# Performance work log

Measured on AMD Instinct MI355X. Metric: run time of the kernel, lower is better.

## Reference

```python
import math
import numpy as np
import jax, jax.numpy as jnp

C = 8  # hidden multiplicity (num_channels)
B, N = 4, 4096

# ---------- real Wigner 3j (e3nn convention: Frobenius norm 1) ----------

def _su2_cg(l1, l2, l3):
    f = math.factorial
    def cg(m1, m2, m3):
        if m1 + m2 != m3:
            return 0.0
        pref = math.sqrt((2 * l3 + 1) * f(l3 + l1 - l2) * f(l3 - l1 + l2) * f(l1 + l2 - l3) / f(l1 + l2 + l3 + 1))
        pref *= math.sqrt(f(l3 + m3) * f(l3 - m3) * f(l1 - m1) * f(l1 + m1) * f(l2 - m2) * f(l2 + m2))
        s = 0.0
        for k in range(l1 + l2 - l3 + 1):
            d = [k, l1 + l2 - l3 - k, l1 - m1 - k, l2 + m2 - k, l3 - l2 + m1 + k, l3 - l1 - m2 + k]
            if min(d) < 0:
                continue
            s += (-1.0) ** k / np.prod([float(f(x)) for x in d])
        return pref * s
    out = np.zeros((2 * l1 + 1, 2 * l2 + 1, 2 * l3 + 1))
    for i, m1 in enumerate(range(-l1, l1 + 1)):
        for j, m2 in enumerate(range(-l2, l2 + 1)):
            for k, m3 in enumerate(range(-l3, l3 + 1)):
                out[i, j, k] = cg(m1, m2, m3)
    return out

def _q_real_to_complex(l):
    q = np.zeros((2 * l + 1, 2 * l + 1), dtype=np.complex128)
    rs2 = 1.0 / math.sqrt(2.0)
    for m in range(-l, 0):
        q[l + m, l + abs(m)] = rs2
        q[l + m, l - abs(m)] = -1j * rs2
    q[l, l] = 1.0
    for m in range(1, l + 1):
        q[l + m, l + abs(m)] = (-1) ** m * rs2
        q[l + m, l - abs(m)] = 1j * (-1) ** m * rs2
    return (-1j) ** l * q

def _w3j(l1, l2, l3):
    Q1, Q2, Q3 = _q_real_to_complex(l1), _q_real_to_complex(l2), _q_real_to_complex(l3)
    Cc = _su2_cg(l1, l2, l3).astype(np.complex128)
    Cr = np.real(np.einsum('ij,kl,mn,ikm->jln', Q1, Q2, np.conj(Q3), Cc))
    return (Cr / np.linalg.norm(Cr)).astype(np.float32)

# tensor-product paths (selection rules for 4e/6e inputs, 0e/2e SH, 4e/6e outputs)
VAL_PATHS = [(4, 0, 4), (4, 2, 4), (6, 2, 4), (4, 2, 6), (6, 0, 6), (6, 2, 6)]
OUT_PATHS = [(4, 4, 4), (4, 6, 4), (6, 4, 4), (6, 6, 4), (4, 4, 6), (4, 6, 6), (6, 4, 6), (6, 6, 6)]
# path normalization ('element'): fan-in = 3*C for tp_val outputs, 4*C^2 for tp_out outputs
W3J_VAL = [jnp.asarray(_w3j(*p) * math.sqrt((2 * p[2] + 1) / (3.0 * C))) for p in VAL_PATHS]
W3J_OUT = [jnp.asarray(_w3j(*p) * math.sqrt((2 * p[2] + 1) / (4.0 * C * C))) for p in OUT_PATHS]


def _forward(feat, sh_lr, log_s, pos_w, pos_b, w_lin_in, w_val, w_out, w_lin_out):
    b, n, _ = feat.shape
    f4, f6 = feat[..., :9], feat[..., 9:]                      # 1x4e, 1x6e
    f4n = f4 / jnp.maximum(jnp.linalg.norm(f4, axis=-1, keepdims=True), 1e-12)
    f6n = f6 / jnp.maximum(jnp.linalg.norm(f6, axis=-1, keepdims=True), 1e-12)
    s4, s6 = jnp.exp(log_s[0]), jnp.exp(log_s[1])
    scores = s4 * jnp.einsum('bnd,bmd->bnm', f4n, f4n) + s6 * jnp.einsum('bnd,bmd->bnm', f6n, f6n)
    pb = sh_lr @ pos_w + pos_b                                 # (N,)
    scores = scores + (pb[:, None] + pb[None, :])[None]
    attn = jax.nn.softmax(scores.astype(jnp.float32), axis=-1).astype(feat.dtype)

    h4 = f4[:, :, None, :] * w_lin_in[0][None, None, :, None]  # (B,N,C,9)
    h6 = f6[:, :, None, :] * w_lin_in[1][None, None, :, None]  # (B,N,C,13)

    y = {0: sh_lr[:, :1], 2: sh_lr[:, 1:]}                     # (N,1), (N,5)
    hx = {4: h4, 6: h6}
    v = {4: jnp.zeros((b, n, C, 9), feat.dtype), 6: jnp.zeros((b, n, C, 13), feat.dtype)}
    for p, (l1, l2, l3) in enumerate(VAL_PATHS):
        v[l3] = v[l3] + jnp.einsum('bnui,nj,ijk,uw->bnwk', hx[l1], y[l2], W3J_VAL[p], w_val[p])
    vals = jnp.concatenate([v[4].reshape(b, n, 9 * C), v[6].reshape(b, n, 13 * C)], axis=-1)

    ctx = jnp.einsum('bnm,bmd->bnd', attn, vals)               # (B,N,22C)
    cx = {4: ctx[..., :9 * C].reshape(b, n, C, 9), 6: ctx[..., 9 * C:].reshape(b, n, C, 13)}
    o = {4: jnp.zeros((b, n, C, 9), feat.dtype), 6: jnp.zeros((b, n, C, 13), feat.dtype)}
    for p, (l1, l2, l3) in enumerate(OUT_PATHS):
        o[l3] = o[l3] + jnp.einsum('bnui,bnvj,ijk,uvw->bnwk', hx[l1], cx[l2], W3J_OUT[p], w_out[p])

    inv_sc = 1.0 / math.sqrt(C)                                # lin_out fan_in = C
    d4 = jnp.einsum('bnui,u->bni', o[4], w_lin_out[0]) * inv_sc
    d6 = jnp.einsum('bnui,u->bni', o[6], w_lin_out[1]) * inv_sc
    return jnp.concatenate([d4, d6], axis=-1)                  # (B,N,22)


def setup_inputs() -> dict:
    key = jax.random.key(0)
    ks = jax.random.split(key, 8)
    feat = jax.random.normal(ks[0], (B, N, 22), jnp.float32)
    sh_lr = jax.random.normal(ks[1], (N, 6), jnp.float32)
    log_s = jnp.array([math.log(1.0 / 3.0), math.log(1.0 / math.sqrt(13.0))], jnp.float32)
    pos_w = 0.01 * jax.random.normal(ks[2], (6,), jnp.float32)
    pos_b = jnp.zeros((), jnp.float32)
    w_lin_in = jax.random.normal(ks[3], (2, C), jnp.float32)
    w_val = jax.random.normal(ks[4], (6, C, C), jnp.float32)
    w_out = jax.random.normal(ks[5], (8, C, C, C), jnp.float32)
    w_lin_out = jax.random.normal(ks[6], (2, C), jnp.float32)
    return dict(feat=feat, sh_lr=sh_lr, log_s=log_s, pos_w=pos_w, pos_b=pos_b,
                w_lin_in=w_lin_in, w_val=w_val, w_out=w_out, w_lin_out=w_lin_out)


def reference(feat, sh_lr, log_s, pos_w, pos_b, w_lin_in, w_val, w_out, w_lin_out):
    return _forward(feat, sh_lr, log_s, pos_w, pos_b, w_lin_in, w_val, w_out, w_lin_out)
```

## Files before the change

kernel.cpp:

```cpp
#include <hip/hip_runtime.h>
#include <cmath>

#define NN 4096
#define BB 4
#define CCH 8

#define OFF_W3JVAL 0
#define OFF_W3JOUT 2688
#define OFF_CTX0   13568
#define CTXS       1572864
#define OFFB_KGH   25220096ULL
#define OFFB_KGL   26268672ULL
#define OFFB_VG    27317248ULL
#define OFFB_WBH   30462976ULL
#define OFFB_WBL   30493696ULL

typedef short s16x8 __attribute__((ext_vector_type(8)));
typedef _Float16 f16x8 __attribute__((ext_vector_type(8)));
typedef float f32x4 __attribute__((ext_vector_type(4)));
typedef unsigned int u32x4 __attribute__((ext_vector_type(4)));
typedef unsigned int u32x2 __attribute__((ext_vector_type(2)));

static __device__ __forceinline__ unsigned short f2bf(float x){
  unsigned u = __float_as_uint(x);
  return (unsigned short)((u + 0x7FFFu + ((u >> 16) & 1u)) >> 16);
}
static __device__ __forceinline__ float bf2f(unsigned short h){
  return __uint_as_float(((unsigned)h) << 16);
}
static __device__ __forceinline__ unsigned pk2r(float v){
  unsigned short h = f2bf(v);
  unsigned short l = f2bf(v - bf2f(h));
  return ((unsigned)l << 16) | (unsigned)h;
}
static __device__ __forceinline__ unsigned short f2h(float x){
  return __builtin_bit_cast(unsigned short, (_Float16)x);
}
static __device__ __forceinline__ void unpk(u32x4 a, u32x4 b, s16x8& h, s16x8& l){
  u32x4 hw = { __builtin_amdgcn_perm(a[1],a[0],0x05040100u),
               __builtin_amdgcn_perm(a[3],a[2],0x05040100u),
               __builtin_amdgcn_perm(b[1],b[0],0x05040100u),
               __builtin_amdgcn_perm(b[3],b[2],0x05040100u)};
  u32x4 lw = { __builtin_amdgcn_perm(a[1],a[0],0x07060302u),
               __builtin_amdgcn_perm(a[3],a[2],0x07060302u),
               __builtin_amdgcn_perm(b[1],b[0],0x07060302u),
               __builtin_amdgcn_perm(b[3],b[2],0x07060302u)};
  h = __builtin_bit_cast(s16x8, hw);
  l = __builtin_bit_cast(s16x8, lw);
}

static __device__ __forceinline__ void qentf(int l, int r, int c, float& re, float& im){
  re=0.f; im=0.f;
  float s = ((l&3)==2)? -1.f : 1.f;
  const float rs2 = 0.70710678118654752440f;
  if(r < l){
    if(c == 2*l - r) re = s*rs2;
    else if(c == r)  im = -s*rs2;
  } else if(r == l){
    if(c == l) re = s;
  } else {
    float sg = ((r-l)&1)? -1.f : 1.f;
    if(c == r) re = s*sg*rs2;
    else if(c == 2*l - r) im = s*sg*rs2;
  }
}
__global__ __launch_bounds__(512) void k_tab(float* __restrict__ Wv, float* __restrict__ Wo){
  __shared__ float Ccf[2197];
  __shared__ float red[512];
  __shared__ double factS[20];
  int t = threadIdx.x;
  int p = blockIdx.x;
  if(t==0){
    double f=1.0; factS[0]=1.0;
    for(int i=1;i<20;i++){ f*=(double)i; factS[i]=f; }
  }
  const int L1[14]={4,4,6,4,6,6, 4,4,6,6,4,4,6,6};
  const int L2[14]={0,2,2,2,0,2, 4,6,4,6,4,6,4,6};
  const int L3[14]={4,4,4,6,6,6, 4,4,4,4,6,6,6,6};
  const int OFF[14]={0,81,486,1071,1656,1825, 0,729,1782,2835,4356,5409,6930,8451};
  int l1=L1[p], l2=L2[p], l3=L3[p];
  int d1=2*l1+1, d2=2*l2+1, d3=2*l3+1;
  int tot = d1*d2*d3;
  float* dst = (p<6) ? (Wv+OFF[p]) : (Wo+OFF[p]);
  float scale = (p<6) ? sqrtf((2.f*l3+1.f)/24.f) : sqrtf((2.f*l3+1.f)/256.f);
  __syncthreads();
  #pragma unroll 1
  for(int e=t; e<tot; e+=512){
    int i = e/(d2*d3), rem = e - i*(d2*d3), j = rem/d3, k = rem - j*d3;
    int m1=i-l1, m2=j-l2, m3=k-l3;
    double v=0.0;
    if(m1+m2==m3){
      double pref = sqrt((2.0*l3+1.0)*factS[l3+l1-l2]*factS[l3-l1+l2]*factS[l1+l2-l3]/factS[l1+l2+l3+1]);
      pref *= sqrt(factS[l3+m3]*factS[l3-m3]*factS[l1-m1]*factS[l1+m1]*factS[l2-m2]*factS[l2+m2]);
      double s=0.0;
      #pragma unroll 1
      for(int kk=0; kk<=l1+l2-l3; kk++){
        int dd0=kk, dd1=l1+l2-l3-kk, dd2=l1-m1-kk, dd3=l2+m2-kk, dd4=l3-l2+m1+kk, dd5=l3-l1-m2+kk;
        int mn=dd0;
        if(dd1<mn)mn=dd1; if(dd2<mn)mn=dd2; if(dd3<mn)mn=dd3; if(dd4<mn)mn=dd4; if(dd5<mn)mn=dd5;
        if(mn<0) continue;
        double prod = factS[dd0]*factS[dd1]*factS[dd2]*factS[dd3]*factS[dd4]*factS[dd5];
        s += ((kk&1)? -1.0:1.0)/prod;
      }
      v = pref*s;
    }
    Ccf[e]=(float)v;
  }
  __syncthreads();
  float nacc=0.f;
  #pragma unroll 1
  for(int e=t; e<tot; e+=512){
    int j = e/(d2*d3), rem = e - j*(d2*d3), l = rem/d3, n = rem - l*d3;
    float re = 0.f;
    #pragma unroll
    for(int ii=0; ii<2; ii++){
      int i = ii ? (2*l1 - j) : j;
      float q1r,q1i; qentf(l1,i,j,q1r,q1i);
      if(ii && i==j){ q1r=0.f; q1i=0.f; }
      #pragma unroll
      for(int kk=0; kk<2; kk++){
        int k = kk ? (2*l2 - l) : l;
        float q2r,q2i; qentf(l2,k,l,q2r,q2i);
        if(kk && k==l){ q2r=0.f; q2i=0.f; }
        float ar = q1r*q2r - q1i*q2i;
        float ai = q1r*q2i + q1i*q2r;
        #pragma unroll
        for(int mm=0; mm<2; mm++){
          int m = mm ? (2*l3 - n) : n;
          float q3r,q3i; qentf(l3,m,n,q3r,q3i);
          if(mm && m==n){ q3r=0.f; q3i=0.f; }
          float coef = ar*q3r + ai*q3i;
          re = fmaf(coef, Ccf[(i*d2+k)*d3+m], re);
        }
      }
    }
    dst[e]=re;
    nacc = fmaf(re,re,nacc);
  }
  red[t]=nacc;
  __syncthreads();
  #pragma unroll 1
  for(int s=256;s>0;s>>=1){
    if(t<s) red[t]+=red[t+s];
    __syncthreads();
  }
  float c = scale/sqrtf(red[0]);
  #pragma unroll 1
  for(int e=t; e<tot; e+=512) dst[e]*=c;
}

__global__ void k_weights(const float* __restrict__ wli, const float* __restrict__ wval,
                          const float* __restrict__ wout, const float* __restrict__ wlo,
                          const float* __restrict__ Wv,
                          unsigned short* __restrict__ WBH, unsigned short* __restrict__ WBL){
  __shared__ float bws[48];
  __shared__ float scs[64];
  __shared__ float As[24];
  int t = threadIdx.x;
  if(t<48){
    const int val_l1[6]={0,0,1,0,1,1};
    int p=t>>3, w=t&7;
    float s=0.f;
    for(int u=0;u<8;u++) s = fmaf(wli[val_l1[p]*8+u], wval[(p*8+u)*8+w], s);
    bws[t]=s;
  }
  {
    const int out_l1[8]={0,0,1,1,0,0,1,1};
    const int out_l3[8]={0,0,0,0,1,1,1,1};
    int p=t>>3, v=t&7;
    float s=0.f;
    for(int u=0;u<8;u++){
      float a=wli[out_l1[p]*8+u];
      for(int w=0;w<8;w++) s = fmaf(wout[((p*8+u)*8+v)*8+w]*a, wlo[out_l3[p]*8+w], s);
    }
    scs[t]=s*0.35355339059327373f;
  }
  __syncthreads();
  if(t<24){
    int p=t/3, i3=t-3*p;
    int vp = (p&1)*3 + i3;
    float s=0.f;
    for(int w=0;w<8;w++) s = fmaf(scs[p*8+w], bws[vp*8+w], s);
    As[t]=s;
  }
  __syncthreads();
  int base = blockIdx.x*960;
  for(int k=0;k<15;k++){
    int cell = base + k*64 + t;
    int f = cell/160, c = cell - f*160;
    float v = 0.f;
    if(f < 88 && c < 132){
      int seg = f/22, off = f - seg*22;
      int even = (off < 9);
      int p = 2*seg + (even?0:1);
      int jo = even ? off : off-9;
      int l1, i, jj;
      if(c < 54){ l1=4; i=c/6; jj=c-6*i; }
      else { int cc=c-54; l1=6; i=cc/6; jj=cc-6*i; }
      if(even){
        if(l1==4 && jj==0)      v = As[p*3+0]*Wv[i*9+jo];
        else if(l1==4)          v = As[p*3+1]*Wv[81+(i*5+jj-1)*9+jo];
        else if(jj>=1)          v = As[p*3+2]*Wv[486+(i*5+jj-1)*9+jo];
      } else {
        if(l1==4 && jj>=1)      v = As[p*3+0]*Wv[1071+(i*5+jj-1)*13+jo];
        else if(l1==6 && jj==0) v = As[p*3+1]*Wv[1656+i*13+jo];
        else if(l1==6)          v = As[p*3+2]*Wv[1825+(i*5+jj-1)*13+jo];
      }
    } else if(f==88 && c==132){
      v = 1.0f;
    }
    unsigned short h = f2bf(v);
    WBH[cell] = h;
    WBL[cell] = f2bf(v - bf2f(h));
  }
}

__launch_bounds__(128)
__global__ void k_prep(const float* __restrict__ feat, const float* __restrict__ sh,
                       const float* __restrict__ log_s, const float* __restrict__ pos_w,
                       const float* __restrict__ pos_b,
                       const unsigned short* __restrict__ WBH,
                       const unsigned short* __restrict__ WBL,
                       unsigned short* __restrict__ Kgh, unsigned short* __restrict__ Kgl,
                       unsigned short* __restrict__ Vg){
  __shared__ __align__(16) unsigned int Pbuf[16*164];
  __shared__ unsigned int Po[96*17];
  __shared__ float epbs[16];
  int tid = threadIdx.x;
  int w2 = tid >> 6, lane = tid & 63;
  int lm = lane & 15, quad = lane >> 4;
  int seg = w2*4 + quad;
  int panel = blockIdx.x >> 2, mt = blockIdx.x & 3;
  int idxp = panel*64 + mt*16 + lm;
  int n = idxp & (NN-1);
  const float* fp = feat + (size_t)idxp*22;
  const float* shp = sh + n*6;
  float f[22];
  #pragma unroll
  for(int c=0;c<22;c++) f[c]=fp[c];
  float y[6];
  #pragma unroll
  for(int j=0;j<6;j++) y[j]=shp[j];
  if(tid<16){
    float pb = pos_b[0];
    #pragma unroll
    for(int j=0;j<6;j++) pb = fmaf(y[j], pos_w[j], pb);
    epbs[lm] = __expf(pb);
    float n4=0.f, n6=0.f;
    #pragma unroll
    for(int c=0;c<9;c++) n4 += f[c]*f[c];
    #pragma unroll
    for(int c=9;c<22;c++) n6 += f[c]*f[c];
    n4 = fmaxf(sqrtf(n4), 1e-12f);
    n6 = fmaxf(sqrtf(n6), 1e-12f);
    float s4 = __expf(log_s[0]), s6 = __expf(log_s[1]);
    float a4 = sqrtf(s4)/n4, a6 = sqrtf(s6)/n6;
    unsigned short* kph = Kgh + (size_t)idxp*32;
    unsigned short* kpl = Kgl + (size_t)idxp*32;
    #pragma unroll
    for(int c=0;c<22;c++){
      float qv = f[c] * (c<9 ? a4 : a6);
      unsigned short h = f2bf(qv);
      kph[c]=h; kpl[c]=f2bf(qv - bf2f(h));
    }
    #pragma unroll
    for(int c=22;c<32;c++){ kph[c]=0; kpl[c]=0; }
  }
  #pragma unroll
  for(int j4=0;j4<5;j4++){
    u32x4 wv;
    #pragma unroll
    for(int e=0;e<4;e++){
      int c = seg*20 + j4*4 + e;
      float pv;
      if(c<54){ int i=c/6, jj=c-6*i; pv = f[i]*y[jj]; }
      else if(c<132){ int cc=c-54; int i=cc/6, jj=cc-6*i; pv = f[9+i]*y[jj]; }
      else if(c==132) pv = 1.0f;
      else pv = 0.0f;
      wv[e] = pk2r(pv);
    }
    *(u32x4*)&Pbuf[lm*164 + seg*20 + j4*4] = wv;
  }
  __syncthreads();
  f32x4 acc[3];
  #pragma unroll
  for(int ft=0;ft<3;ft++)
    #pragma unroll
    for(int i=0;i<4;i++) acc[ft][i]=0.f;
  for(int kc=0;kc<5;kc++){
    const u32x4* ap = (const u32x4*)&Pbuf[lm*164 + kc*32 + quad*8];
    s16x8 Ah, Al;
    unpk(ap[0], ap[1], Ah, Al);
    #pragma unroll
    for(int ft=0;ft<3;ft++){
      int ftg = w2*3 + ft;
      size_t bo = (size_t)(ftg*16+lm)*160 + kc*32 + quad*8;
      s16x8 Bh = *(const s16x8*)(WBH + bo);
      s16x8 Bl = *(const s16x8*)(WBL + bo);
      f32x4 a = acc[ft];
      a = __builtin_amdgcn_mfma_f32_16x16x32_bf16(Al, Bl, a, 0,0,0);
      a = __builtin_amdgcn_mfma_f32_16x16x32_bf16(Al, Bh, a, 0,0,0);
      a = __builtin_amdgcn_mfma_f32_16x16x32_bf16(Ah, Bl, a, 0,0,0);
      a = __builtin_amdgcn_mfma_f32_16x16x32_bf16(Ah, Bh, a, 0,0,0);
      acc[ft] = a;
    }
  }
  #pragma unroll
  for(int r=0;r<4;r++){
    float e = epbs[quad*4 + r];
    #pragma unroll
    for(int ft=0;ft<3;ft++){
      int ftg = w2*3 + ft;
      Po[(ftg*16+lm)*17 + quad*4 + r] = (unsigned)f2h(acc[ft][r]*e);
    }
  }
  __syncthreads();
  unsigned int* vO32 = (unsigned int*)(Vg + (size_t)panel*96*64);
  #pragma unroll
  for(int wv=0; wv<6; wv++){
    int idx2 = wv*128 + tid;
    int g = idx2 >> 3, j = idx2 & 7;
    unsigned lo = Po[g*17 + 2*j] & 0xFFFFu;
    unsigned hi = Po[g*17 + 2*j + 1] & 0xFFFFu;
    vO32[g*32 + mt*8 + j] = lo | (hi<<16);
  }
}

#define LDSK  0
#define LDSKL 4096
#define LDSV  8192
#define BUFB  20480
__global__ __launch_bounds__(512)
__attribute__((amdgpu_waves_per_eu(4, 4)))
void k_attn(const unsigned short* __restrict__ Kgh,
            const unsigned short* __restrict__ Kgl,
            const unsigned short* __restrict__ Vg,
            float* __restrict__ ctx0){
  __shared__ __align__(16) unsigned char lds[73728];
  int tid = threadIdx.x;
  int lane = tid & 63, w = tid >> 6;
  int lm = lane & 15, quad = lane >> 4;
  int blk = blockIdx.x;
  int b = blk & 3, kh = (blk>>2)&3, qb = blk >> 4;
  const unsigned short* KhB = Kgh + (size_t)b*NN*32;
  const unsigned short* KlB = Kgl + (size_t)b*NN*32;
  const unsigned short* VB  = Vg  + (size_t)b*64*96*64;
  float* ctx = ctx0 + (size_t)kh*CTXS + (size_t)b*NN*96;
  int qrow = qb*128 + w*16 + lm;

  s16x8 qh, ql;
  { size_t ro = (size_t)qrow*32 + (size_t)quad*8;
    qh = *(const s16x8*)(KhB + ro);
    ql = *(const s16x8*)(KlB + ro); }

  int kro = lm*64 + ((quad ^ ((lm>>1)&3))<<4);
  int vr0 = lm*128 + (((0*4+quad) ^ (lm&7))<<4);
  int vr1 = lm*128 + (((1*4+quad) ^ (lm&7))<<4);

  int dofs[3], sofs[3], sreg[3];
  #pragma unroll
  for(int rep=0;rep<3;rep++){
    int g = tid + 512*rep;
    if(g < 512){
      int gk = g & 255;
      int row = gk>>2, col = gk&3;
      int t = row>>4, rr = row&15;
      int kact = 32*(t&1) + 8*(rr>>2) + 4*(t>>1) + (rr&3);
      sreg[rep] = (g<256)? 0 : 1;
      sofs[rep] = kact*64 + col*16;
      dofs[rep] = ((g<256)? LDSK : LDSKL) + row*64 + ((col ^ ((row>>1)&3))<<4);
    }
    else if(g < 1280){ int gv=g-512; sreg[rep]=2; sofs[rep]=gv*16;
      dofs[rep] = LDSV + (gv>>3)*128 + (((gv&7) ^ ((gv>>3)&7))<<4); }
    else { sreg[rep]=-1; sofs[rep]=0; dofs[rep]=0; }
  }

  f32x4 acc[6];
  #pragma unroll
  for(int ft=0;ft<6;ft++)
    #pragma unroll
    for(int i=0;i<4;i++) acc[ft][i]=0.f;

  u32x4 stg0, stg1, stg2;

#define MFB(A,Bv,C) __builtin_amdgcn_mfma_f32_16x16x32_bf16(A,Bv,C,0,0,0)
#define MFH(A,Bv,C) __builtin_amdgcn_mfma_f32_16x16x32_f16(A,Bv,C,0,0,0)

#define STG_ISSUE(T) { \
  const char* kb_ = (const char*)(KhB + (size_t)(kh*16+(T))*2048); \
  const char* lb_ = (const char*)(KlB + (size_t)(kh*16+(T))*2048); \
  const char* vb_ = (const char*)(VB  + (size_t)(kh*16+(T))*6144); \
  { const char* sp_ = (sreg[0]==0)? kb_ : (sreg[0]==1)? lb_ : vb_; \
    stg0 = *(const u32x4*)(sp_ + sofs[0]); } \
  { const char* sp_ = (sreg[1]==0)? kb_ : (sreg[1]==1)? lb_ : vb_; \
    stg1 = *(const u32x4*)(sp_ + sofs[1]); } \
  if(sreg[2]>=0){ stg2 = *(const u32x4*)(vb_ + sofs[2]); } }

#define STG_WRITE(BN) { \
  *(u32x4*)&lds[(BN)*BUFB + dofs[0]] = stg0; \
  *(u32x4*)&lds[(BN)*BUFB + dofs[1]] = stg1; \
  if(sreg[2]>=0){ *(u32x4*)&lds[(BN)*BUFB + dofs[2]] = stg2; } }

#define COMPUTE(B) { \
  unsigned Wt[4][2]; \
  _Pragma("unroll") \
  for(int kt=0;kt<4;kt++){ \
    s16x8 kfh = *(const s16x8*)&lds[(B)*BUFB + LDSK  + kt*1024 + kro]; \
    s16x8 kfl = *(const s16x8*)&lds[(B)*BUFB + LDSKL + kt*1024 + kro]; \
    f32x4 s_ = {0.f,0.f,0.f,0.f}; \
    s_ = MFB(kfl, qh, s_); \
    s_ = MFB(kfh, ql, s_); \
    s_ = MFB(kfh, qh, s_); \
    Wt[kt][0] = (unsigned)f2h(__expf(s_[0])) | ((unsigned)f2h(__expf(s_[1]))<<16); \
    Wt[kt][1] = (unsigned)f2h(__expf(s_[2])) | ((unsigned)f2h(__expf(s_[3]))<<16); \
  } \
  _Pragma("unroll") \
  for(int c=0;c<2;c++){ \
    u32x4 paw = {Wt[c][0], Wt[c][1], Wt[c+2][0], Wt[c+2][1]}; \
    f16x8 PA = __builtin_bit_cast(f16x8, paw); \
    int vro_ = c ? vr1 : vr0; \
    _Pragma("unroll") \
    for(int ft=0;ft<6;ft++){ \
      f16x8 vf = *(const f16x8*)&lds[(B)*BUFB + LDSV + ft*2048 + vro_]; \
      acc[ft] = MFH(PA, vf, acc[ft]); } \
  } }

  STG_ISSUE(0);
  STG_WRITE(0);
  __syncthreads();

  #pragma unroll 1
  for(int tp=0; tp<8; tp++){
    int t0 = 2*tp;
    STG_ISSUE(t0+1);
    COMPUTE(0);
    STG_WRITE(1);
    __syncthreads();
    if(t0+2 < 16){ STG_ISSUE(t0+2); }
    COMPUTE(1);
    if(t0+2 < 16){ STG_WRITE(0); }
    __syncthreads();
  }

#undef MFB
#undef MFH
#undef STG_ISSUE
#undef STG_WRITE
#undef COMPUTE

  #pragma unroll
  for(int ft=0;ft<6;ft++){
    int col = ft*16 + lm;
    #pragma unroll
    for(int r=0;r<4;r++){
      int row = qb*128 + w*16 + quad*4 + r;
      ctx[(size_t)row*96 + col] = acc[ft][r];
    }
  }
}

__launch_bounds__(256, 4)
__global__ void k_out(const float* __restrict__ feat, const float* __restrict__ ctxA,
                      const float* __restrict__ w3jout, float* __restrict__ out){
  __shared__ float gbuf[16*45];
  __shared__ float fbuf[16*24];
  __shared__ float dls[4*64*13];
  __shared__ float inv[16];
  int tid = threadIdx.x;
  int typ = blockIdx.x & 1;
  int n0 = (blockIdx.x>>1)*16;
  int gc0 = typ*44;
  for(int i=tid;i<16*44;i+=256){
    int pt=i/44, c=i-pt*44;
    const float* base = ctxA + (size_t)(n0+pt)*96 + gc0 + c;
    gbuf[pt*45+c] = base[0]+base[CTXS]+base[2*CTXS]+base[3*CTXS];
  }
  for(int i=tid;i<16*22;i+=256){
    int pt=i/22, c=i-pt*22;
    fbuf[pt*24+c] = feat[(size_t)(n0+pt)*22+c];
  }
  if(tid<16){
    const float* bd = ctxA + (size_t)(n0+tid)*96 + 88;
    inv[tid] = 1.0f/(bd[0]+bd[CTXS]+bd[2*CTXS]+bd[3*CTXS]);
  }
  __syncthreads();
  int lane = tid&63, w = tid>>6;
  int pt = lane&15, sub = lane>>4;
  float fR[13], gR[13], d[13];
  {
    int FB = (w&2)?9:0;
    int fn = (w&2)?13:9;
    #pragma unroll 13
    for(int i=0;i<13;i++) fR[i] = (i<fn) ? fbuf[pt*24 + FB + i] : 0.f;
    int GBl = (w==0)?0:(w==1)?9:(w==2)?22:31;
    int jn = (w&1)?13:9;
    #pragma unroll 13
    for(int j=0;j<13;j++) gR[j] = (j<jn) ? gbuf[pt*45 + GBl + j] : 0.f;
  }
  #pragma unroll 13
  for(int k=0;k<13;k++) d[k]=0.f;

#define PATHR(ID,JD,KD,WO) \
  _Pragma("unroll") \
  for(int ii=0;ii<((ID)+3)/4;ii++){ int i=sub+4*ii; if(i<(ID)){ float fv=fR[i]; \
    _Pragma("unroll") \
    for(int j=0;j<(JD);j++){ float val=fv*gR[j]; \
      const float* wp = w3jout + (WO) + (i*(JD)+j)*(KD); \
      _Pragma("unroll") \
      for(int k=0;k<(KD);k++) d[k] = fmaf(val, wp[k], d[k]); } } }

  int pcase = typ*4 + w;
  switch(pcase){
    case 0: PATHR(9,9,9, 0)       break;
    case 1: PATHR(9,13,9, 729)    break;
    case 2: PATHR(13,9,9, 1782)   break;
    case 3: PATHR(13,13,9, 2835)  break;
    case 4: PATHR(9,9,13, 4356)   break;
    case 5: PATHR(9,13,13, 5409)  break;
    case 6: PATHR(13,9,13, 6930)  break;
    default:PATHR(13,13,13, 8451) break;
  }
#undef PATHR
  {
    float* dp = &dls[(w*64+lane)*13];
    #pragma unroll 13
    for(int k=0;k<13;k++) dp[k]=d[k];
  }
  __syncthreads();
  {
    int KD = typ?13:9;
    int kb = typ?9:0;
    int pt2 = tid&15, kc = tid>>4;
    if(kc < KD){
      float s = 0.f;
      #pragma unroll
      for(int ww=0;ww<4;ww++)
        #pragma unroll
        for(int ss=0;ss<4;ss++)
          s += dls[(ww*64 + ss*16 + pt2)*13 + kc];
      out[(size_t)(n0+pt2)*22 + kb + kc] = s*inv[pt2];
    }
  }
}

extern "C" void kernel_launch(void* const* d_in, const int* in_sizes, int n_in,
                              void* d_out, int out_size, void* d_ws, size_t ws_size,
                              hipStream_t stream){
  (void)in_sizes; (void)n_in; (void)out_size; (void)ws_size;
  const float* feat =(const float*)d_in[0];
  const float* sh   =(const float*)d_in[1];
  const float* log_s=(const float*)d_in[2];
  const float* pos_w=(const float*)d_in[3];
  const float* pos_b=(const float*)d_in[4];
  const float* wli  =(const float*)d_in[5];
  const float* wval =(const float*)d_in[6];
  const float* wout =(const float*)d_in[7];
  const float* wlo  =(const float*)d_in[8];
  float* outp=(float*)d_out;
  float* wsf=(float*)d_ws;

  unsigned short* Kgh=(unsigned short*)((char*)d_ws + OFFB_KGH);
  unsigned short* Kgl=(unsigned short*)((char*)d_ws + OFFB_KGL);
  unsigned short* Vg =(unsigned short*)((char*)d_ws + OFFB_VG);
  unsigned short* WBH=(unsigned short*)((char*)d_ws + OFFB_WBH);
  unsigned short* WBL=(unsigned short*)((char*)d_ws + OFFB_WBL);

  hipLaunchKernelGGL(k_tab, dim3(14), dim3(512), 0, stream,
                     wsf+OFF_W3JVAL, wsf+OFF_W3JOUT);
  hipLaunchKernelGGL(k_weights, dim3(16), dim3(64), 0, stream,
                     wli, wval, wout, wlo, wsf+OFF_W3JVAL, WBH, WBL);
  hipLaunchKernelGGL(k_prep, dim3(1024), dim3(128), 0, stream,
                     feat, sh, log_s, pos_w, pos_b, WBH, WBL,
                     Kgh, Kgl, Vg);
  hipLaunchKernelGGL(k_attn, dim3(512), dim3(512), 0, stream,
                     Kgh, Kgl, Vg, wsf+OFF_CTX0);
  hipLaunchKernelGGL(k_out, dim3(2048), dim3(256), 0, stream,
                     feat, wsf+OFF_CTX0, wsf+OFF_W3JOUT, outp);
}
```

Before: 177.8 us.

## Process two query tiles per wave in attention kernel to reuse staged K/V

Each wave now handles 32 query rows (two 16-row tiles) instead of 16. The K and V fragments loaded from LDS are reused across both tiles, and the grid is halved to 256 blocks, so global-to-LDS staging traffic per query is halved. Accumulator and register use roughly doubles, so the occupancy hint drops from 4 to 2 waves per EU. The LDS allocation is also trimmed to the two buffers actually used. The cost is lower occupancy and fewer blocks to spread across the CUs.

Result: no change. 176.8 us (-0.6%).

```diff
diff --git a/kernel.cpp b/kernel.cpp
--- a/kernel.cpp
+++ b/kernel.cpp
@@ -331,12 +331,12 @@
 #define LDSV  8192
 #define BUFB  20480
 __global__ __launch_bounds__(512)
-__attribute__((amdgpu_waves_per_eu(4, 4)))
+__attribute__((amdgpu_waves_per_eu(2, 2)))
 void k_attn(const unsigned short* __restrict__ Kgh,
             const unsigned short* __restrict__ Kgl,
             const unsigned short* __restrict__ Vg,
             float* __restrict__ ctx0){
-  __shared__ __align__(16) unsigned char lds[73728];
+  __shared__ __align__(16) unsigned char lds[2*BUFB];
   int tid = threadIdx.x;
   int lane = tid & 63, w = tid >> 6;
   int lm = lane & 15, quad = lane >> 4;
@@ -346,12 +346,14 @@
   const unsigned short* KlB = Kgl + (size_t)b*NN*32;
   const unsigned short* VB  = Vg  + (size_t)b*64*96*64;
   float* ctx = ctx0 + (size_t)kh*CTXS + (size_t)b*NN*96;
-  int qrow = qb*128 + w*16 + lm;
-
-  s16x8 qh, ql;
-  { size_t ro = (size_t)qrow*32 + (size_t)quad*8;
-    qh = *(const s16x8*)(KhB + ro);
-    ql = *(const s16x8*)(KlB + ro); }
+
+  s16x8 qh[2], ql[2];
+  #pragma unroll
+  for(int q2=0;q2<2;q2++){
+    size_t ro = (size_t)(qb*256 + w*32 + q2*16 + lm)*32 + (size_t)quad*8;
+    qh[q2] = *(const s16x8*)(KhB + ro);
+    ql[q2] = *(const s16x8*)(KlB + ro);
+  }
 
   int kro = lm*64 + ((quad ^ ((lm>>1)&3))<<4);
   int vr0 = lm*128 + (((0*4+quad) ^ (lm&7))<<4);
@@ -375,11 +377,13 @@
     else { sreg[rep]=-1; sofs[rep]=0; dofs[rep]=0; }
   }
 
-  f32x4 acc[6];
-  #pragma unroll
-  for(int ft=0;ft<6;ft++)
-    #pragma unroll
-    for(int i=0;i<4;i++) acc[ft][i]=0.f;
+  f32x4 acc[2][6];
+  #pragma unroll
+  for(int q2=0;q2<2;q2++)
+    #pragma unroll
+    for(int ft=0;ft<6;ft++)
+      #pragma unroll
+      for(int i=0;i<4;i++) acc[q2][ft][i]=0.f;
 
   u32x4 stg0, stg1, stg2;
 
@@ -402,27 +406,33 @@
   if(sreg[2]>=0){ *(u32x4*)&lds[(BN)*BUFB + dofs[2]] = stg2; } }
 
 #define COMPUTE(B) { \
-  unsigned Wt[4][2]; \
+  unsigned Wt[2][4][2]; \
   _Pragma("unroll") \
   for(int kt=0;kt<4;kt++){ \
     s16x8 kfh = *(const s16x8*)&lds[(B)*BUFB + LDSK  + kt*1024 + kro]; \
     s16x8 kfl = *(const s16x8*)&lds[(B)*BUFB + LDSKL + kt*1024 + kro]; \
-    f32x4 s_ = {0.f,0.f,0.f,0.f}; \
-    s_ = MFB(kfl, qh, s_); \
-    s_ = MFB(kfh, ql, s_); \
-    s_ = MFB(kfh, qh, s_); \
-    Wt[kt][0] = (unsigned)f2h(__expf(s_[0])) | ((unsigned)f2h(__expf(s_[1]))<<16); \
-    Wt[kt][1] = (unsigned)f2h(__expf(s_[2])) | ((unsigned)f2h(__expf(s_[3]))<<16); \
+    _Pragma("unroll") \
+    for(int q2=0;q2<2;q2++){ \
+      f32x4 s_ = {0.f,0.f,0.f,0.f}; \
+      s_ = MFB(kfl, qh[q2], s_); \
+      s_ = MFB(kfh, ql[q2], s_); \
+      s_ = MFB(kfh, qh[q2], s_); \
+      Wt[q2][kt][0] = (unsigned)f2h(__expf(s_[0])) | ((unsigned)f2h(__expf(s_[1]))<<16); \
+      Wt[q2][kt][1] = (unsigned)f2h(__expf(s_[2])) | ((unsigned)f2h(__expf(s_[3]))<<16); \
+    } \
   } \
   _Pragma("unroll") \
   for(int c=0;c<2;c++){ \
-    u32x4 paw = {Wt[c][0], Wt[c][1], Wt[c+2][0], Wt[c+2][1]}; \
-    f16x8 PA = __builtin_bit_cast(f16x8, paw); \
+    u32x4 paw0 = {Wt[0][c][0], Wt[0][c][1], Wt[0][c+2][0], Wt[0][c+2][1]}; \
+    u32x4 paw1 = {Wt[1][c][0], Wt[1][c][1], Wt[1][c+2][0], Wt[1][c+2][1]}; \
+    f16x8 PA0 = __builtin_bit_cast(f16x8, paw0); \
+    f16x8 PA1 = __builtin_bit_cast(f16x8, paw1); \
     int vro_ = c ? vr1 : vr0; \
     _Pragma("unroll") \
     for(int ft=0;ft<6;ft++){ \
       f16x8 vf = *(const f16x8*)&lds[(B)*BUFB + LDSV + ft*2048 + vro_]; \
-      acc[ft] = MFH(PA, vf, acc[ft]); } \
+      acc[0][ft] = MFH(PA0, vf, acc[0][ft]); \
+      acc[1][ft] = MFH(PA1, vf, acc[1][ft]); } \
   } }
 
   STG_ISSUE(0);
@@ -449,12 +459,15 @@
 #undef COMPUTE
 
   #pragma unroll
-  for(int ft=0;ft<6;ft++){
-    int col = ft*16 + lm;
-    #pragma unroll
-    for(int r=0;r<4;r++){
-      int row = qb*128 + w*16 + quad*4 + r;
-      ctx[(size_t)row*96 + col] = acc[ft][r];
+  for(int q2=0;q2<2;q2++){
+    #pragma unroll
+    for(int ft=0;ft<6;ft++){
+      int col = ft*16 + lm;
+      #pragma unroll
+      for(int r=0;r<4;r++){
+        int row = qb*256 + w*32 + q2*16 + quad*4 + r;
+        ctx[(size_t)row*96 + col] = acc[q2][ft][r];
+      }
     }
   }
 }
@@ -572,7 +585,7 @@
   hipLaunchKernelGGL(k_prep, dim3(1024), dim3(128), 0, stream,
                      feat, sh, log_s, pos_w, pos_b, WBH, WBL,
                      Kgh, Kgl, Vg);
-  hipLaunchKernelGGL(k_attn, dim3(512), dim3(512), 0, stream,
+  hipLaunchKernelGGL(k_attn, dim3(256), dim3(512), 0, stream,
                      Kgh, Kgl, Vg, wsf+OFF_CTX0);
   hipLaunchKernelGGL(k_out, dim3(2048), dim3(256), 0, stream,
                      feat, wsf+OFF_CTX0, wsf+OFF_W3JOUT, outp);
```
